# Kernel tuning notes

Hardware: AMD Instinct MI355X
Metric: run time of the kernel (lower is better)

Reference implementation:

```python
import jax, jax.numpy as jnp
import numpy as np

E_ROUTER = 32      # routed experts with real FFNs
ZERO_E = 8         # zero-experts (identity skip)
TOP_K = 4
ROUTED_SCALE = 2.5


def setup_inputs() -> dict:
    key = jax.random.key(0)
    k1, k2, k3, k4, k5 = jax.random.split(key, 5)
    T, H, I = 2048, 1024, 512
    N = E_ROUTER + ZERO_E
    return {
        "hidden_states": jax.random.normal(k1, (T, H), jnp.float32),
        "router_w": jax.random.normal(k2, (N, H), jnp.float32) * 0.02,            # classifier weight [N, H]
        "e_score_correction_bias": jax.random.normal(k3, (N,), jnp.float32) * 0.01,
        "w13": jax.random.normal(k4, (E_ROUTER, 2 * I, H), jnp.float32) * 0.02,   # gate+up per expert
        "w2": jax.random.normal(k5, (E_ROUTER, H, I), jnp.float32) * 0.02,        # down proj per expert
    }


def reference(hidden_states, router_w, e_score_correction_bias, w13, w2):
    T, H = hidden_states.shape
    I = w2.shape[-1]

    # --- router (LongcatFlashTopkRouter) ---
    logits = hidden_states @ router_w.T                         # [T, N]
    scores = jax.nn.softmax(logits, axis=-1)
    biased = scores + e_score_correction_bias[None, :]
    _, topk_ids = jax.lax.top_k(biased, TOP_K)                  # indices chosen on biased scores
    topk_w = jnp.take_along_axis(scores, topk_ids, axis=-1) * ROUTED_SCALE  # weights from unbiased scores

    # --- zero experts: ids >= E_ROUTER contribute weight * x directly ---
    zero_mask = topk_ids >= E_ROUTER
    zero_total = jnp.sum(jnp.where(zero_mask, topk_w, 0.0), axis=-1, keepdims=True)  # [T,1]
    zero_expert_output = hidden_states * zero_total
    topk_w = jnp.where(zero_mask, 0.0, topk_w)
    topk_ids = jnp.where(zero_mask, 0, topk_ids)

    # --- combine weights per (token, expert): scatter-add of topk weights ---
    combine = jnp.zeros((T, E_ROUTER), jnp.float32).at[
        jnp.arange(T)[:, None], topk_ids
    ].add(topk_w)                                               # [T, E]

    # --- experts: swiglu FFN per expert (dense form of grouped GEMM; zero combine
    #     weights make it mathematically identical to dispatch/compute/combine) ---
    gate_up = jnp.einsum('th,eih->eti', hidden_states, w13)     # [E, T, 2I]
    gate, up = gate_up[..., :I], gate_up[..., I:]
    h = jax.nn.silu(gate) * up                                  # [E, T, I]
    expert_out = jnp.einsum('eti,ehi->eth', h, w2)              # [E, T, H]
    routed = jnp.einsum('eth,te->th', expert_out, combine)      # [T, H]

    return routed + zero_expert_output
```

## Files before the change

kernel.cpp:

```cpp
#include <hip/hip_runtime.h>
#include <math.h>

#define TT 2048
#define HH 1024
#define NE 40
#define ER 32
#define II 512
#define TOPK 4
#define RSCALE 2.5f
#define MAXW 64

typedef __bf16 bf16x8 __attribute__((ext_vector_type(8)));
typedef float f32x4 __attribute__((ext_vector_type(4)));

__global__ __launch_bounds__(256) void k_router(const float* __restrict__ hidden,
                                                const float* __restrict__ rw,
                                                const float* __restrict__ bias,
                                                float* __restrict__ out,
                                                int* __restrict__ tok4_id,
                                                float* __restrict__ tok4_w,
                                                __bf16* __restrict__ hid_bf) {
  int lane = threadIdx.x & 63;
  int t = blockIdx.x * 4 + (threadIdx.x >> 6);
  const float* hrow = hidden + (size_t)t * HH;
  float4 hv[4];
  #pragma unroll
  for (int c = 0; c < 4; c++) hv[c] = *(const float4*)(hrow + c * 256 + lane * 4);

  float mylg = -INFINITY;
  for (int e = 0; e < NE; e++) {
    const float* wrow = rw + (size_t)e * HH;
    float p = 0.f;
    #pragma unroll
    for (int c = 0; c < 4; c++) {
      float4 w4 = *(const float4*)(wrow + c * 256 + lane * 4);
      p += hv[c].x * w4.x + hv[c].y * w4.y + hv[c].z * w4.z + hv[c].w * w4.w;
    }
    #pragma unroll
    for (int off = 32; off; off >>= 1) p += __shfl_xor(p, off);
    if (lane == e) mylg = p;
  }
  float m = mylg;
  #pragma unroll
  for (int off = 32; off; off >>= 1) m = fmaxf(m, __shfl_xor(m, off));
  float p = (lane < NE) ? expf(mylg - m) : 0.f;
  float s = p;
  #pragma unroll
  for (int off = 32; off; off >>= 1) s += __shfl_xor(s, off);
  float score = p / s;
  float v = (lane < NE) ? score + bias[lane] : -INFINITY;
  int ids[TOPK]; float wv[TOPK];
  #pragma unroll
  for (int k = 0; k < TOPK; k++) {
    float mv = v;
    int mi = (lane < NE) ? lane : 63;
    #pragma unroll
    for (int off = 32; off; off >>= 1) {
      float ov = __shfl_xor(mv, off);
      int oi = __shfl_xor(mi, off);
      if (ov > mv || (ov == mv && oi < mi)) { mv = ov; mi = oi; }
    }
    ids[k] = mi;
    wv[k] = RSCALE * __shfl(score, mi);
    if (lane == mi) v = -INFINITY;
  }
  float zt = 0.f;
  #pragma unroll
  for (int k = 0; k < TOPK; k++) if (ids[k] >= ER) zt += wv[k];
  if (lane == 0) {
    #pragma unroll
    for (int k = 0; k < TOPK; k++) {
      tok4_id[t * TOPK + k] = ids[k];
      tok4_w[t * TOPK + k] = wv[k];
    }
  }
  #pragma unroll
  for (int c = 0; c < 4; c++) {
    int j = c * 256 + lane * 4;
    float4 h4 = hv[c];
    *(float4*)(out + (size_t)t * HH + j) =
        make_float4(h4.x * zt, h4.y * zt, h4.z * zt, h4.w * zt);
    union { __bf16 h[4]; uint2 u; } pk;
    pk.h[0] = (__bf16)h4.x; pk.h[1] = (__bf16)h4.y;
    pk.h[2] = (__bf16)h4.z; pk.h[3] = (__bf16)h4.w;
    *(uint2*)(hid_bf + (size_t)t * HH + j) = pk.u;
  }
}

__global__ __launch_bounds__(256) void k_scanscatter(const int* __restrict__ tok4_id,
                                                     const float* __restrict__ tok4_w,
                                                     int* __restrict__ cnt,
                                                     int* __restrict__ offs,
                                                     int* __restrict__ wl_e,
                                                     int* __restrict__ wl_m0,
                                                     int* __restrict__ nwork,
                                                     int* __restrict__ pair_tok,
                                                     float* __restrict__ pair_w) {
  __shared__ int scnt[32];
  __shared__ int scur[32];
  int tid = threadIdx.x;
  if (tid < 32) scnt[tid] = 0;
  __syncthreads();
  int ids[32]; float wv[32];
  #pragma unroll
  for (int i = 0; i < 32; i++) {
    int idx = i * 256 + tid;
    ids[i] = tok4_id[idx];
    wv[i] = tok4_w[idx];
    if (ids[i] < ER) atomicAdd(&scnt[ids[i]], 1);
  }
  __syncthreads();
  if (tid < 64) {
    int lane = tid;
    int c = (lane < ER) ? scnt[lane] : 0;
    int ts = (c + 255) >> 8;
    int ps = c, pt = ts;
    #pragma unroll
    for (int off = 1; off < 32; off <<= 1) {
      int v1 = __shfl_up(ps, off);
      int v2 = __shfl_up(pt, off);
      if (lane >= off) { ps += v1; pt += v2; }
    }
    if (lane < ER) {
      int o = ps - c;
      offs[lane] = o; cnt[lane] = c; scur[lane] = o;
      int tb = pt - ts;
      for (int i = 0; i < ts; i++) { wl_e[tb + i] = lane; wl_m0[tb + i] = i * 256; }
    }
    if (lane == 31) *nwork = pt;
  }
  __syncthreads();
  #pragma unroll
  for (int i = 0; i < 32; i++) {
    if (ids[i] < ER) {
      int pos = atomicAdd(&scur[ids[i]], 1);
      pair_tok[pos] = (i * 256 + tid) >> 2;
      pair_w[pos] = wv[i];
    }
  }
}

__global__ __launch_bounds__(256) void k_w13(const __bf16* __restrict__ hid_bf,
                                             const float* __restrict__ w13,
                                             const int* __restrict__ cnt,
                                             const int* __restrict__ offs,
                                             const int* __restrict__ pair_tok,
                                             const int* __restrict__ wl_e,
                                             const int* __restrict__ wl_m0,
                                             const int* __restrict__ nwork,
                                             __bf16* __restrict__ h_buf) {
  int bx = blockIdx.x;
  if (bx >= *nwork) return;
  int e = wl_e[bx], m0w = wl_m0[bx];
  int M = cnt[e] - m0w; if (M > 256) M = 256;
  int base = offs[e] + m0w;
  int n0 = blockIdx.y * 32;

  __shared__ __bf16 As[256][72];
  __shared__ __bf16 Bs[64][72];
  __shared__ int tl[256];

  int tid = threadIdx.x;
  int lane = tid & 63, w = tid >> 6;
  int quad = lane >> 4, rr = lane & 15;

  tl[tid] = pair_tok[base + ((tid < M) ? tid : 0)];

  const float* wg_base = w13 + (size_t)e * (2 * II) * HH + (size_t)n0 * HH;
  const float* wu_base = w13 + (size_t)e * (2 * II) * HH + (size_t)(II + n0) * HH;

  f32x4 accg[4][2] = {};
  f32x4 accu[4][2] = {};
  __syncthreads();

  for (int k0 = 0; k0 < HH; k0 += 64) {
    #pragma unroll
    for (int p = 0; p < 8; p++) {
      int s = p * 256 + tid;
      int r = s >> 3, c = (s & 7) * 8;
      *(uint4*)&As[r][c] = *(const uint4*)(hid_bf + (size_t)tl[r] * HH + k0 + c);
    }
    #pragma unroll
    for (int p = 0; p < 4; p++) {
      int s = p * 256 + tid;
      int r = s >> 4, c = (s & 15) * 4;
      const float* src = ((r < 32) ? (wg_base + (size_t)r * HH)
                                   : (wu_base + (size_t)(r - 32) * HH)) + k0 + c;
      float4 v = *(const float4*)src;
      union { __bf16 h[4]; uint2 u; } pk;
      pk.h[0] = (__bf16)v.x; pk.h[1] = (__bf16)v.y;
      pk.h[2] = (__bf16)v.z; pk.h[3] = (__bf16)v.w;
      *(uint2*)&Bs[r][c] = pk.u;
    }
    __syncthreads();
    #pragma unroll
    for (int ks = 0; ks < 2; ks++) {
      int kb = ks * 32 + quad * 8;
      bf16x8 a[4], bg[2], bu[2];
      #pragma unroll
      for (int i = 0; i < 4; i++) a[i] = *(const bf16x8*)&As[w * 64 + i * 16 + rr][kb];
      #pragma unroll
      for (int j = 0; j < 2; j++) {
        bg[j] = *(const bf16x8*)&Bs[j * 16 + rr][kb];
        bu[j] = *(const bf16x8*)&Bs[32 + j * 16 + rr][kb];
      }
      #pragma unroll
      for (int i = 0; i < 4; i++)
        #pragma unroll
        for (int j = 0; j < 2; j++) {
          accg[i][j] = __builtin_amdgcn_mfma_f32_16x16x32_bf16(a[i], bg[j], accg[i][j], 0, 0, 0);
          accu[i][j] = __builtin_amdgcn_mfma_f32_16x16x32_bf16(a[i], bu[j], accu[i][j], 0, 0, 0);
        }
    }
    __syncthreads();
  }
  #pragma unroll
  for (int i = 0; i < 4; i++)
    #pragma unroll
    for (int j = 0; j < 2; j++)
      #pragma unroll
      for (int l = 0; l < 4; l++) {
        int m = w * 64 + i * 16 + quad * 4 + l;
        if (m < M) {
          float g = accg[i][j][l], u = accu[i][j][l];
          float hv = g / (1.f + expf(-g)) * u;
          h_buf[(size_t)(base + m) * II + n0 + j * 16 + rr] = (__bf16)hv;
        }
      }
}

__global__ __launch_bounds__(256) void k_w2(const __bf16* __restrict__ h_buf,
                                            const float* __restrict__ w2,
                                            const int* __restrict__ cnt,
                                            const int* __restrict__ offs,
                                            const int* __restrict__ pair_tok,
                                            const float* __restrict__ pair_w,
                                            const int* __restrict__ wl_e,
                                            const int* __restrict__ wl_m0,
                                            const int* __restrict__ nwork,
                                            float* __restrict__ out) {
  int bx = blockIdx.x;
  if (bx >= *nwork) return;
  int e = wl_e[bx], m0w = wl_m0[bx];
  int M = cnt[e] - m0w; if (M > 256) M = 256;
  int base = offs[e] + m0w;
  int h0 = blockIdx.y * 64;

  __shared__ __bf16 As[256][72];
  __shared__ __bf16 Bs[64][72];
  __shared__ int tl[256];
  __shared__ float wl[256];

  int tid = threadIdx.x;
  int lane = tid & 63, w = tid >> 6;
  int quad = lane >> 4, rr = lane & 15;

  {
    int ok = tid < M;
    tl[tid] = ok ? pair_tok[base + tid] : 0;
    wl[tid] = ok ? pair_w[base + tid] : 0.f;
  }
  const __bf16* h_base = h_buf + (size_t)base * II;
  const float* w_base = w2 + (size_t)e * HH * II + (size_t)h0 * II;

  f32x4 acc[4][4] = {};
  __syncthreads();

  for (int k0 = 0; k0 < II; k0 += 64) {
    #pragma unroll
    for (int p = 0; p < 8; p++) {
      int s = p * 256 + tid;
      int r = s >> 3, c = (s & 7) * 8;
      *(uint4*)&As[r][c] = *(const uint4*)(h_base + (size_t)r * II + k0 + c);
    }
    #pragma unroll
    for (int p = 0; p < 4; p++) {
      int s = p * 256 + tid;
      int r = s >> 4, c = (s & 15) * 4;
      float4 v = *(const float4*)(w_base + (size_t)r * II + k0 + c);
      union { __bf16 h[4]; uint2 u; } pk;
      pk.h[0] = (__bf16)v.x; pk.h[1] = (__bf16)v.y;
      pk.h[2] = (__bf16)v.z; pk.h[3] = (__bf16)v.w;
      *(uint2*)&Bs[r][c] = pk.u;
    }
    __syncthreads();
    #pragma unroll
    for (int ks = 0; ks < 2; ks++) {
      int kb = ks * 32 + quad * 8;
      bf16x8 a[4], b[4];
      #pragma unroll
      for (int i = 0; i < 4; i++) a[i] = *(const bf16x8*)&As[w * 64 + i * 16 + rr][kb];
      #pragma unroll
      for (int j = 0; j < 4; j++) b[j] = *(const bf16x8*)&Bs[j * 16 + rr][kb];
      #pragma unroll
      for (int i = 0; i < 4; i++)
        #pragma unroll
        for (int j = 0; j < 4; j++)
          acc[i][j] = __builtin_amdgcn_mfma_f32_16x16x32_bf16(a[i], b[j], acc[i][j], 0, 0, 0);
    }
    __syncthreads();
  }
  #pragma unroll
  for (int i = 0; i < 4; i++)
    #pragma unroll
    for (int l = 0; l < 4; l++) {
      int m = w * 64 + i * 16 + quad * 4 + l;
      if (m < M) {
        int t = tl[m];
        float wp = wl[m];
        #pragma unroll
        for (int j = 0; j < 4; j++)
          atomicAdd(&out[(size_t)t * HH + h0 + j * 16 + rr], acc[i][j][l] * wp);
      }
    }
}

extern "C" void kernel_launch(void* const* d_in, const int* in_sizes, int n_in,
                              void* d_out, int out_size, void* d_ws, size_t ws_size,
                              hipStream_t stream) {
  const float* hidden = (const float*)d_in[0];
  const float* rw     = (const float*)d_in[1];
  const float* bias   = (const float*)d_in[2];
  const float* w13    = (const float*)d_in[3];
  const float* w2     = (const float*)d_in[4];
  float* out = (float*)d_out;

  int* ws_i = (int*)d_ws;
  int* tok4_id = ws_i;
  float* tok4_w = (float*)(tok4_id + TT * TOPK);
  int* pair_tok = (int*)(tok4_w + TT * TOPK);
  float* pair_w = (float*)(pair_tok + TT * TOPK);
  int* cnt = (int*)(pair_w + TT * TOPK);
  int* offs = cnt + 32;
  int* wl_e = offs + 32;
  int* wl_m0 = wl_e + 64;
  int* nwork = wl_m0 + 64;
  __bf16* hid_bf = (__bf16*)(nwork + 64);
  __bf16* h_buf = hid_bf + (size_t)TT * HH;

  k_router<<<dim3(TT / 4), dim3(256), 0, stream>>>(hidden, rw, bias, out,
                                                   tok4_id, tok4_w, hid_bf);
  k_scanscatter<<<dim3(1), dim3(256), 0, stream>>>(tok4_id, tok4_w, cnt, offs,
                                                   wl_e, wl_m0, nwork, pair_tok, pair_w);
  k_w13<<<dim3(MAXW, 16), dim3(256), 0, stream>>>(hid_bf, w13, cnt, offs, pair_tok,
                                                  wl_e, wl_m0, nwork, h_buf);
  k_w2<<<dim3(MAXW, 16), dim3(256), 0, stream>>>(h_buf, w2, cnt, offs, pair_tok, pair_w,
                                                 wl_e, wl_m0, nwork, out);
}
```

Before: 341.9 us.

## Register-prefetch next K tile in expert GEMMs to overlap loads with MFMA

Both expert GEMM kernels (w13 and w2) now load the next K-slice of activations and weights into registers while the current tile's MFMAs run, then store them to shared memory at the top of the next iteration. Row pointers, including the gathered token rows in k_w13, are computed once before the loop, so the per-iteration shared-memory token lookup goes away. This is meant to hide global-memory latency behind compute. The cost is extra register pressure from 12 vector prefetch registers per thread, which may reduce occupancy.

```diff
diff --git a/kernel.cpp b/kernel.cpp
--- a/kernel.cpp
+++ b/kernel.cpp
@@ -158,41 +158,57 @@
 
   __shared__ __bf16 As[256][72];
   __shared__ __bf16 Bs[64][72];
-  __shared__ int tl[256];
 
   int tid = threadIdx.x;
   int lane = tid & 63, w = tid >> 6;
   int quad = lane >> 4, rr = lane & 15;
 
-  tl[tid] = pair_tok[base + ((tid < M) ? tid : 0)];
-
   const float* wg_base = w13 + (size_t)e * (2 * II) * HH + (size_t)n0 * HH;
   const float* wu_base = w13 + (size_t)e * (2 * II) * HH + (size_t)(II + n0) * HH;
 
+  int arow = tid >> 3, acol = (tid & 7) * 8;
+  int brow = tid >> 4, bcol = (tid & 15) * 4;
+  const __bf16* aptr[8];
+  #pragma unroll
+  for (int p = 0; p < 8; p++) {
+    int r = p * 32 + arow;
+    int tok = pair_tok[base + ((r < M) ? r : 0)];
+    aptr[p] = hid_bf + (size_t)tok * HH + acol;
+  }
+  const float* bptr[4];
+  #pragma unroll
+  for (int p = 0; p < 4; p++) {
+    int r = p * 16 + brow;
+    bptr[p] = ((r < 32) ? (wg_base + (size_t)r * HH)
+                        : (wu_base + (size_t)(r - 32) * HH)) + bcol;
+  }
+
+  uint4 pa[8]; float4 pb[4];
+  #pragma unroll
+  for (int p = 0; p < 8; p++) pa[p] = *(const uint4*)(aptr[p]);
+  #pragma unroll
+  for (int p = 0; p < 4; p++) pb[p] = *(const float4*)(bptr[p]);
+
   f32x4 accg[4][2] = {};
   f32x4 accu[4][2] = {};
-  __syncthreads();
 
   for (int k0 = 0; k0 < HH; k0 += 64) {
     #pragma unroll
-    for (int p = 0; p < 8; p++) {
-      int s = p * 256 + tid;
-      int r = s >> 3, c = (s & 7) * 8;
-      *(uint4*)&As[r][c] = *(const uint4*)(hid_bf + (size_t)tl[r] * HH + k0 + c);
-    }
+    for (int p = 0; p < 8; p++) *(uint4*)&As[p * 32 + arow][acol] = pa[p];
     #pragma unroll
     for (int p = 0; p < 4; p++) {
-      int s = p * 256 + tid;
-      int r = s >> 4, c = (s & 15) * 4;
-      const float* src = ((r < 32) ? (wg_base + (size_t)r * HH)
-                                   : (wu_base + (size_t)(r - 32) * HH)) + k0 + c;
-      float4 v = *(const float4*)src;
       union { __bf16 h[4]; uint2 u; } pk;
-      pk.h[0] = (__bf16)v.x; pk.h[1] = (__bf16)v.y;
-      pk.h[2] = (__bf16)v.z; pk.h[3] = (__bf16)v.w;
-      *(uint2*)&Bs[r][c] = pk.u;
+      pk.h[0] = (__bf16)pb[p].x; pk.h[1] = (__bf16)pb[p].y;
+      pk.h[2] = (__bf16)pb[p].z; pk.h[3] = (__bf16)pb[p].w;
+      *(uint2*)&Bs[p * 16 + brow][bcol] = pk.u;
     }
     __syncthreads();
+    if (k0 + 64 < HH) {
+      #pragma unroll
+      for (int p = 0; p < 8; p++) pa[p] = *(const uint4*)(aptr[p] + k0 + 64);
+      #pragma unroll
+      for (int p = 0; p < 4; p++) pb[p] = *(const float4*)(bptr[p] + k0 + 64);
+    }
     #pragma unroll
     for (int ks = 0; ks < 2; ks++) {
       int kb = ks * 32 + quad * 8;
@@ -212,7 +228,7 @@
           accu[i][j] = __builtin_amdgcn_mfma_f32_16x16x32_bf16(a[i], bu[j], accu[i][j], 0, 0, 0);
         }
     }
-    __syncthreads();
+    if (k0 + 64 < HH) __syncthreads();
   }
   #pragma unroll
   for (int i = 0; i < 4; i++)
@@ -263,27 +279,37 @@
   const __bf16* h_base = h_buf + (size_t)base * II;
   const float* w_base = w2 + (size_t)e * HH * II + (size_t)h0 * II;
 
+  int arow = tid >> 3, acol = (tid & 7) * 8;
+  int brow = tid >> 4, bcol = (tid & 15) * 4;
+  const __bf16* aptr = h_base + (size_t)arow * II + acol;
+  const float* bptr = w_base + (size_t)brow * II + bcol;
+
+  uint4 pa[8]; float4 pb[4];
+  #pragma unroll
+  for (int p = 0; p < 8; p++) pa[p] = *(const uint4*)(aptr + (size_t)p * 32 * II);
+  #pragma unroll
+  for (int p = 0; p < 4; p++) pb[p] = *(const float4*)(bptr + (size_t)p * 16 * II);
+
   f32x4 acc[4][4] = {};
   __syncthreads();
 
   for (int k0 = 0; k0 < II; k0 += 64) {
     #pragma unroll
-    for (int p = 0; p < 8; p++) {
-      int s = p * 256 + tid;
-      int r = s >> 3, c = (s & 7) * 8;
-      *(uint4*)&As[r][c] = *(const uint4*)(h_base + (size_t)r * II + k0 + c);
-    }
+    for (int p = 0; p < 8; p++) *(uint4*)&As[p * 32 + arow][acol] = pa[p];
     #pragma unroll
     for (int p = 0; p < 4; p++) {
-      int s = p * 256 + tid;
-      int r = s >> 4, c = (s & 15) * 4;
-      float4 v = *(const float4*)(w_base + (size_t)r * II + k0 + c);
       union { __bf16 h[4]; uint2 u; } pk;
-      pk.h[0] = (__bf16)v.x; pk.h[1] = (__bf16)v.y;
-      pk.h[2] = (__bf16)v.z; pk.h[3] = (__bf16)v.w;
-      *(uint2*)&Bs[r][c] = pk.u;
+      pk.h[0] = (__bf16)pb[p].x; pk.h[1] = (__bf16)pb[p].y;
+      pk.h[2] = (__bf16)pb[p].z; pk.h[3] = (__bf16)pb[p].w;
+      *(uint2*)&Bs[p * 16 + brow][bcol] = pk.u;
     }
     __syncthreads();
+    if (k0 + 64 < II) {
+      #pragma unroll
+      for (int p = 0; p < 8; p++) pa[p] = *(const uint4*)(aptr + (size_t)p * 32 * II + k0 + 64);
+      #pragma unroll
+      for (int p = 0; p < 4; p++) pb[p] = *(const float4*)(bptr + (size_t)p * 16 * II + k0 + 64);
+    }
     #pragma unroll
     for (int ks = 0; ks < 2; ks++) {
       int kb = ks * 32 + quad * 8;
@@ -298,7 +324,7 @@
         for (int j = 0; j < 4; j++)
           acc[i][j] = __builtin_amdgcn_mfma_f32_16x16x32_bf16(a[i], b[j], acc[i][j], 0, 0, 0);
     }
-    __syncthreads();
+    if (k0 + 64 < II) __syncthreads();
   }
   #pragma unroll
   for (int i = 0; i < 4; i++)
```

After: 494.1 us. 44.5% more time.
